# Kernel tuning notes

Measured on AMD Instinct MI355X. Metric: run time of the kernel, lower is better.

Reference implementation:

```python
import jax, jax.numpy as jnp
import numpy as np

B, L, D_MODEL = 2, 1024, 1024
D_INNER = 2 * D_MODEL
D_STATE = 16
DT_RANK = 64


def _pow2_scale(var, eps=1e-9):
    v = var + eps
    s = jnp.ones_like(v)
    s = jnp.where(v >= 4.0, 0.5, s)
    s = jnp.where(v >= 16.0, 0.25, s)
    s = jnp.where(v >= 64.0, 0.125, s)
    s = jnp.where(v >= 256.0, 0.0625, s)
    s = jnp.where(v >= 1024.0, 0.03125, s)
    s = jnp.where(v >= 4096.0, 0.015625, s)
    s = jnp.where(v >= 16384.0, 0.0078125, s)
    s = jnp.where(v >= 65536.0, 0.00390625, s)
    s = jnp.where(v < 1.0, 1.0, s)
    s = jnp.where(v < 0.25, 2.0, s)
    s = jnp.where(v < 0.0625, 4.0, s)
    s = jnp.where(v < 0.015625, 8.0, s)
    return s


def _rsqrt_newton(y, num_iters=3):
    y = jnp.clip(y, 1e-6, 1e6)
    r = jnp.where(y > 16.0, 0.125, 0.5)
    r = jnp.where(y > 64.0, 0.0625, r)
    r = jnp.where(y > 256.0, 0.03125, r)
    r = jnp.where(y < 4.0, 1.0, r)
    r = jnp.where(y < 1.0, 2.0, r)
    r = jnp.where(y < 0.25, 4.0, r)
    for _ in range(num_iters):
        r = r * (1.5 - 0.5 * y * r * r)
        r = jnp.clip(r, 1e-6, 1000.0)
    return r


def _sqrt_rational(y, num_iters=3):
    y_safe = jnp.clip(y, 1e-6, 1e6)
    return jnp.clip(y_safe * _rsqrt_newton(y_safe, num_iters), 0.0, 1000.0)


def _squareplus(x, num_iters=3):
    return 0.5 * (x + _sqrt_rational(x * x + 4.0, num_iters))


def _sigmoid_alg(z):
    return 0.5 + 0.5 * z / (1.0 + jnp.abs(z))


def _ste_clamp(x, lo, hi):
    return x + jax.lax.stop_gradient(jnp.clip(x, lo, hi) - x)


def _bitshift_norm(x, gamma):
    x = x - jnp.mean(x, axis=-1, keepdims=True)           # module-level centering
    xc = x - jnp.mean(x, axis=-1, keepdims=True)          # function-level centering
    var = jnp.mean(xc * xc, axis=-1, keepdims=True)
    return xc * _pow2_scale(var) * gamma


def _dyadic_scan(u, decay):
    # u, decay: [B, L, DN]; h_t = h_{t-1} * decay_t + u_t
    u_t = jnp.moveaxis(u, 1, 0)       # [L, B, DN]
    d_t = jnp.moveaxis(decay, 1, 0)
    h0 = jnp.zeros((u.shape[0], u.shape[2]), u.dtype)

    def step(h, inp):
        ut, dt = inp
        h = h * dt + ut
        return h, h

    _, hs = jax.lax.scan(step, h0, (u_t, d_t))
    return jnp.moveaxis(hs, 0, 1)     # [B, L, DN]


def setup_inputs() -> dict:
    key = jax.random.key(0)
    ks = jax.random.split(key, 6)
    s = 0.02
    return {
        'hidden_states': jax.random.normal(ks[0], (B, L, D_MODEL), jnp.float32),
        'gamma': jnp.ones((D_MODEL,), jnp.float32),
        'W_in': jax.random.normal(ks[1], (2 * D_INNER, D_MODEL), jnp.float32) * s,
        'conv_w': jax.random.normal(ks[2], (D_INNER, 1, 4), jnp.float32) * 0.3,
        'conv_b': jnp.zeros((D_INNER,), jnp.float32),
        'W_x': jax.random.normal(ks[3], (DT_RANK + 2 * D_STATE, D_INNER), jnp.float32) * s,
        'W_dt': jax.random.normal(ks[4], (D_INNER, DT_RANK), jnp.float32) * s,
        'W_out': jax.random.normal(ks[5], (D_MODEL, D_INNER), jnp.float32) * s,
        'base_decay_nums': jnp.full((D_INNER, D_STATE), 28000.0, jnp.float32),
        'res_gate': jnp.full((1,), 0.01, jnp.float32),
        'decay_shifts': jnp.full((D_INNER, D_STATE), 15.0, jnp.float32),
    }


def reference(hidden_states, gamma, W_in, conv_w, conv_b, W_x, W_dt, W_out,
              base_decay_nums, res_gate, decay_shifts):
    residual = hidden_states
    hs = _bitshift_norm(hidden_states, gamma)

    xz = jnp.clip(hs @ W_in.T, -100.0, 100.0)             # [B,L,2*d_inner]
    x, z = jnp.split(xz, 2, axis=-1)

    # depthwise conv1d, kernel 4, padding 3, keep first L steps
    xT = jnp.transpose(x, (0, 2, 1))                      # [B, d_inner, L]
    xT = jax.lax.conv_general_dilated(
        xT, conv_w, window_strides=(1,), padding=[(3, 3)],
        feature_group_count=D_INNER,
        dimension_numbers=('NCH', 'OIH', 'NCH')) + conv_b[None, :, None]
    x = jnp.transpose(xT, (0, 2, 1))[:, :L]

    x = _squareplus(jnp.clip(x, -50.0, 50.0), 3)

    xp = jnp.clip(x @ W_x.T, -100.0, 100.0)               # [B,L,dt_rank+2*d_state]
    dt = xp[..., :DT_RANK]
    B_ssm = xp[..., DT_RANK:DT_RANK + D_STATE]
    C_ssm = xp[..., DT_RANK + D_STATE:]

    decay_mod = jnp.clip(dt @ W_dt.T, -20.0, 20.0)        # [B,L,d_inner]
    decay_nums = _ste_clamp(base_decay_nums[None, None] + decay_mod[..., None], 0.0, 32000.0)
    dt_val = _ste_clamp(_squareplus(decay_mod, 3) * 0.01, 0.0, 0.1)

    u = (x * dt_val)[..., None] * B_ssm[:, :, None, :]    # [B,L,d_inner,d_state]
    DN = D_INNER * D_STATE
    u_flat = jnp.clip(u.reshape(B, L, DN), -100.0, 100.0)
    dn_flat = decay_nums.reshape(B, L, DN)
    ds_flat = decay_shifts.reshape(DN)[None, None, :]
    decay = dn_flat / jnp.exp2(ds_flat)                   # dyadic decay

    h_flat = _dyadic_scan(u_flat, decay)
    h_flat = jnp.nan_to_num(h_flat, nan=0.0, posinf=100.0, neginf=-100.0)
    h_flat = jnp.clip(h_flat, -1000.0, 1000.0)
    h = h_flat.reshape(B, L, D_INNER, D_STATE)

    y = jnp.clip(jnp.einsum('blds,bls->bld', h, C_ssm), -100.0, 100.0)
    y = y * _sigmoid_alg(z)
    y = jnp.nan_to_num(y, nan=0.0, posinf=50.0, neginf=-50.0)

    out = jnp.clip(y @ W_out.T, -100.0, 100.0)
    return residual + out * res_gate
```

## Files before the change

### kernel.cpp

```cpp
#include <hip/hip_runtime.h>
#include <hip/hip_bf16.h>
#include <math.h>

#define D_MODEL 1024
#define D_INNER 2048
#define D_STATE 16
#define DT_RANK 64
#define LSEQ 1024
#define BATCH 2
#define NTOK (BATCH*LSEQ)
#define NCHUNK 64
#define CLEN 16

typedef __attribute__((ext_vector_type(8))) short bf16x8;
typedef __attribute__((ext_vector_type(4))) float f32x4;

__device__ __forceinline__ float clampf(float v, float lo, float hi){
  return fminf(fmaxf(v, lo), hi);
}
__device__ __forceinline__ unsigned short bfbits(float v){
  return __builtin_bit_cast(unsigned short, __float2bfloat16(v));
}
__device__ __forceinline__ float bf2f(unsigned short u){
  unsigned int x = ((unsigned int)u) << 16;
  return __builtin_bit_cast(float, x);
}

__device__ __forceinline__ float rsqrt_newton3(float y){
  #pragma clang fp contract(off)
  y = clampf(y, 1e-6f, 1e6f);
  float r = 0.5f;
  if (y > 16.f)   r = 0.125f;
  if (y > 64.f)   r = 0.0625f;
  if (y > 256.f)  r = 0.03125f;
  if (y < 4.f)    r = 1.0f;
  if (y < 1.f)    r = 2.0f;
  if (y < 0.25f)  r = 4.0f;
  #pragma unroll
  for (int i = 0; i < 3; ++i){
    r = r * (1.5f - 0.5f * y * r * r);
    r = clampf(r, 1e-6f, 1000.f);
  }
  return r;
}
__device__ __forceinline__ float sqrt_rational3(float y){
  #pragma clang fp contract(off)
  float ys = clampf(y, 1e-6f, 1e6f);
  return clampf(ys * rsqrt_newton3(ys), 0.f, 1000.f);
}
__device__ __forceinline__ float squareplus3(float x){
  #pragma clang fp contract(off)
  return 0.5f * (x + sqrt_rational3(x * x + 4.f));
}

__device__ __forceinline__ float pow2_scale(float var){
  float v = var + 1e-9f;
  float s = 1.f;
  if (v >= 4.f)      s = 0.5f;
  if (v >= 16.f)     s = 0.25f;
  if (v >= 64.f)     s = 0.125f;
  if (v >= 256.f)    s = 0.0625f;
  if (v >= 1024.f)   s = 0.03125f;
  if (v >= 4096.f)   s = 0.015625f;
  if (v >= 16384.f)  s = 0.0078125f;
  if (v >= 65536.f)  s = 0.00390625f;
  if (v < 1.f)       s = 1.f;
  if (v < 0.25f)     s = 2.f;
  if (v < 0.0625f)   s = 4.f;
  if (v < 0.015625f) s = 8.f;
  return s;
}

__device__ __forceinline__ float block_sum(float v, float* sm){
  #pragma unroll
  for (int o = 32; o >= 1; o >>= 1) v += __shfl_xor(v, o, 64);
  __syncthreads();
  if ((threadIdx.x & 63) == 0) sm[threadIdx.x >> 6] = v;
  __syncthreads();
  return sm[0] + sm[1] + sm[2] + sm[3];
}

__global__ __launch_bounds__(256) void norm_kernel(const float* __restrict__ x,
    const float* __restrict__ gamma, unsigned short* __restrict__ out)
{
  __shared__ float sm[4];
  int row = blockIdx.x;
  int t = threadIdx.x;
  float4 v = ((const float4*)(x + (size_t)row * D_MODEL))[t];
  float total = block_sum(v.x + v.y + v.z + v.w, sm);
  float mean1 = total * (1.f / 1024.f);
  v.x -= mean1; v.y -= mean1; v.z -= mean1; v.w -= mean1;
  float total2 = block_sum(v.x + v.y + v.z + v.w, sm);
  float mean2 = total2 * (1.f / 1024.f);
  v.x -= mean2; v.y -= mean2; v.z -= mean2; v.w -= mean2;
  float var = block_sum(v.x*v.x + v.y*v.y + v.z*v.z + v.w*v.w, sm) * (1.f / 1024.f);
  float sc = pow2_scale(var);
  float4 g = ((const float4*)gamma)[t];
  ushort4 o;
  o.x = bfbits(v.x * sc * g.x); o.y = bfbits(v.y * sc * g.y);
  o.z = bfbits(v.z * sc * g.z); o.w = bfbits(v.w * sc * g.w);
  ((ushort4*)(out + (size_t)row * D_MODEL))[t] = o;
}

__global__ __launch_bounds__(256) void cast_bf_kernel(
    const float4* __restrict__ in, ushort4* __restrict__ out, int n4)
{
  int i = blockIdx.x * 256 + threadIdx.x;
  if (i >= n4) return;
  float4 v = in[i];
  ushort4 o;
  o.x = bfbits(v.x); o.y = bfbits(v.y); o.z = bfbits(v.z); o.w = bfbits(v.w);
  out[i] = o;
}

__global__ __launch_bounds__(256) void castpad_wx_kernel(
    const float4* __restrict__ in, ushort4* __restrict__ out)
{
  int i = blockIdx.x * 256 + threadIdx.x;
  if (i >= 65536) return;
  int row = (i * 4) >> 11;
  ushort4 o = make_ushort4(0, 0, 0, 0);
  if (row < 96){
    float4 v = in[i];
    o.x = bfbits(v.x); o.y = bfbits(v.y); o.z = bfbits(v.z); o.w = bfbits(v.w);
  }
  out[i] = o;
}

template<int MT, int EPI>
__global__ __launch_bounds__(256) void gemm_mfma_kernel(
    const unsigned short* __restrict__ A, const unsigned short* __restrict__ Wt,
    float* __restrict__ C, unsigned short* __restrict__ Cb,
    const float* __restrict__ resid, const float* __restrict__ gate,
    int M, int N, int K, int ldc)
{
  constexpr int BM = MT * 32;
  constexpr int ACALLS = (BM * 4) / 256;
  __shared__ unsigned short sA[BM * 32];
  __shared__ unsigned short sB[128 * 32];
  const int tid = threadIdx.x;
  const int w = tid >> 6, l = tid & 63;
  const int wr = w >> 1, wc = w & 1;
  const int m0 = blockIdx.y * BM;
  const int n0 = blockIdx.x * 128;

  const unsigned short* agp[ACALLS];
  int alds[ACALLS];
  #pragma unroll
  for (int i = 0; i < ACALLS; ++i){
    int c = (w * ACALLS + i) * 64 + l;
    int row = c >> 2, kc = c & 3;
    int kcg = kc ^ ((row >> 1) & 3);
    agp[i] = A + (size_t)(m0 + row) * K + kcg * 8;
    alds[i] = __builtin_amdgcn_readfirstlane((w * ACALLS + i) * 1024);
  }
  const unsigned short* bgp[2];
  int blds[2];
  #pragma unroll
  for (int i = 0; i < 2; ++i){
    int c = (w * 2 + i) * 64 + l;
    int row = c >> 2, kc = c & 3;
    int kcg = kc ^ ((row >> 1) & 3);
    bgp[i] = Wt + (size_t)(n0 + row) * K + kcg * 8;
    blds[i] = __builtin_amdgcn_readfirstlane((w * 2 + i) * 1024);
  }
  const int lr = l & 15, kcl = l >> 4;
  const int kc_rd = kcl ^ ((lr >> 1) & 3);
  const int offA = (wr * (MT * 16) + lr) * 32 + kc_rd * 8;
  const int offB = (wc * 64 + lr) * 32 + kc_rd * 8;

  f32x4 acc[MT][4];
  #pragma unroll
  for (int i = 0; i < MT; ++i)
    #pragma unroll
    for (int j = 0; j < 4; ++j)
      acc[i][j] = (f32x4){0.f, 0.f, 0.f, 0.f};

  for (int kk = 0; kk < K; kk += 32){
    #pragma unroll
    for (int i = 0; i < ACALLS; ++i)
      __builtin_amdgcn_global_load_lds(
          (const __attribute__((address_space(1))) unsigned int*)(agp[i]),
          (__attribute__((address_space(3))) unsigned int*)((char*)sA + alds[i]),
          16, 0, 0);
    #pragma unroll
    for (int i = 0; i < 2; ++i)
      __builtin_amdgcn_global_load_lds(
          (const __attribute__((address_space(1))) unsigned int*)(bgp[i]),
          (__attribute__((address_space(3))) unsigned int*)((char*)sB + blds[i]),
          16, 0, 0);
    #pragma unroll
    for (int i = 0; i < ACALLS; ++i) agp[i] += 32;
    #pragma unroll
    for (int i = 0; i < 2; ++i) bgp[i] += 32;
    __syncthreads();
    bf16x8 av[MT], bv[4];
    #pragma unroll
    for (int i = 0; i < MT; ++i)
      av[i] = *(const bf16x8*)(const void*)(sA + offA + i * 512);
    #pragma unroll
    for (int j = 0; j < 4; ++j)
      bv[j] = *(const bf16x8*)(const void*)(sB + offB + j * 512);
    #pragma unroll
    for (int i = 0; i < MT; ++i)
      #pragma unroll
      for (int j = 0; j < 4; ++j)
        acc[i][j] = __builtin_amdgcn_mfma_f32_16x16x32_bf16(av[i], bv[j], acc[i][j], 0, 0, 0);
    __syncthreads();
  }

  float gv = (EPI == 2) ? gate[0] : 0.f;
  const int lq = l >> 4;
  #pragma unroll
  for (int i = 0; i < MT; ++i){
    int rbase = m0 + wr * (MT * 16) + i * 16 + lq * 4;
    #pragma unroll
    for (int j = 0; j < 4; ++j){
      int col = n0 + wc * 64 + j * 16 + lr;
      if (col < N){
        #pragma unroll
        for (int r = 0; r < 4; ++r){
          float v = clampf(acc[i][j][r], -100.f, 100.f);
          size_t idx = (size_t)(rbase + r) * ldc + col;
          if (EPI == 1) Cb[idx] = bfbits(v);
          else          C[idx] = resid[idx] + v * gv;
        }
      }
    }
  }
}

template<int SPLITS>
__global__ __launch_bounds__(256) void gemm2_splitk_kernel(
    const unsigned short* __restrict__ A, const unsigned short* __restrict__ Wt,
    float* __restrict__ Part, int M, int N, int K)
{
  constexpr int BM = 128;
  __shared__ unsigned short sA[BM * 32];
  __shared__ unsigned short sB[128 * 32];
  const int tid = threadIdx.x;
  const int w = tid >> 6, l = tid & 63;
  const int wr = w >> 1, wc = w & 1;
  const int m0 = blockIdx.y * BM;
  const int kseg = K / SPLITS;
  const int kbeg = blockIdx.z * kseg;

  const unsigned short* agp[2];
  int alds[2];
  #pragma unroll
  for (int i = 0; i < 2; ++i){
    int c = (w * 2 + i) * 64 + l;
    int row = c >> 2, kc = c & 3;
    int kcg = kc ^ ((row >> 1) & 3);
    agp[i] = A + (size_t)(m0 + row) * K + kbeg + kcg * 8;
    alds[i] = __builtin_amdgcn_readfirstlane((w * 2 + i) * 1024);
  }
  const unsigned short* bgp[2];
  int blds[2];
  #pragma unroll
  for (int i = 0; i < 2; ++i){
    int c = (w * 2 + i) * 64 + l;
    int row = c >> 2, kc = c & 3;
    int kcg = kc ^ ((row >> 1) & 3);
    bgp[i] = Wt + (size_t)row * K + kbeg + kcg * 8;
    blds[i] = __builtin_amdgcn_readfirstlane((w * 2 + i) * 1024);
  }
  const int lr = l & 15, kcl = l >> 4;
  const int kc_rd = kcl ^ ((lr >> 1) & 3);
  const int offA = (wr * 64 + lr) * 32 + kc_rd * 8;
  const int offB = (wc * 64 + lr) * 32 + kc_rd * 8;

  f32x4 acc[4][4];
  #pragma unroll
  for (int i = 0; i < 4; ++i)
    #pragma unroll
    for (int j = 0; j < 4; ++j)
      acc[i][j] = (f32x4){0.f, 0.f, 0.f, 0.f};

  for (int kk = 0; kk < kseg; kk += 32){
    #pragma unroll
    for (int i = 0; i < 2; ++i){
      __builtin_amdgcn_global_load_lds(
          (const __attribute__((address_space(1))) unsigned int*)(agp[i]),
          (__attribute__((address_space(3))) unsigned int*)((char*)sA + alds[i]),
          16, 0, 0);
      __builtin_amdgcn_global_load_lds(
          (const __attribute__((address_space(1))) unsigned int*)(bgp[i]),
          (__attribute__((address_space(3))) unsigned int*)((char*)sB + blds[i]),
          16, 0, 0);
      agp[i] += 32; bgp[i] += 32;
    }
    __syncthreads();
    bf16x8 av[4], bv[4];
    #pragma unroll
    for (int i = 0; i < 4; ++i)
      av[i] = *(const bf16x8*)(const void*)(sA + offA + i * 512);
    #pragma unroll
    for (int j = 0; j < 4; ++j)
      bv[j] = *(const bf16x8*)(const void*)(sB + offB + j * 512);
    #pragma unroll
    for (int i = 0; i < 4; ++i)
      #pragma unroll
      for (int j = 0; j < 4; ++j)
        acc[i][j] = __builtin_amdgcn_mfma_f32_16x16x32_bf16(av[i], bv[j], acc[i][j], 0, 0, 0);
    __syncthreads();
  }

  float* outz = Part + (size_t)blockIdx.z * M * 96;
  const int lq = l >> 4;
  #pragma unroll
  for (int i = 0; i < 4; ++i){
    int rbase = m0 + wr * 64 + i * 16 + lq * 4;
    #pragma unroll
    for (int j = 0; j < 4; ++j){
      int col = wc * 64 + j * 16 + lr;
      if (col < N){
        #pragma unroll
        for (int r = 0; r < 4; ++r)
          outz[(size_t)(rbase + r) * 96 + col] = acc[i][j][r];
      }
    }
  }
}

template<int SPLITS>
__global__ __launch_bounds__(256) void reduce_xp_kernel(
    const float4* __restrict__ Part, float4* __restrict__ xp, int n4)
{
  int i = blockIdx.x * 256 + threadIdx.x;
  if (i >= n4) return;
  float4 s = Part[i];
  #pragma unroll
  for (int z = 1; z < SPLITS; ++z){
    float4 p = Part[(size_t)z * n4 + i];
    s.x += p.x; s.y += p.y; s.z += p.z; s.w += p.w;
  }
  s.x = clampf(s.x, -100.f, 100.f); s.y = clampf(s.y, -100.f, 100.f);
  s.z = clampf(s.z, -100.f, 100.f); s.w = clampf(s.w, -100.f, 100.f);
  xp[i] = s;
}

__global__ __launch_bounds__(256) void gemm3_kernel(
    const float* __restrict__ A, const float* __restrict__ W,
    unsigned short* __restrict__ Cdm, unsigned short* __restrict__ Cdt,
    int M, int N, int K, int lda, int ldc)
{
  __shared__ float sA[16][68];
  __shared__ float sW[16][68];
  int tid = threadIdx.x;
  int n0 = blockIdx.x * 64;
  int m0 = blockIdx.y * 64;
  int tx = tid & 15, ty = tid >> 4;
  int lrow = tid >> 2, lquad = tid & 3;
  float acc[4][4] = {};
  for (int k0 = 0; k0 < K; k0 += 16){
    float4 a4 = *(const float4*)(A + (size_t)(m0 + lrow) * lda + k0 + lquad * 4);
    float4 w4 = *(const float4*)(W + (size_t)(n0 + lrow) * K + k0 + lquad * 4);
    __syncthreads();
    sA[lquad*4+0][lrow] = a4.x; sA[lquad*4+1][lrow] = a4.y;
    sA[lquad*4+2][lrow] = a4.z; sA[lquad*4+3][lrow] = a4.w;
    sW[lquad*4+0][lrow] = w4.x; sW[lquad*4+1][lrow] = w4.y;
    sW[lquad*4+2][lrow] = w4.z; sW[lquad*4+3][lrow] = w4.w;
    __syncthreads();
    #pragma unroll
    for (int k = 0; k < 16; ++k){
      float4 av = *(const float4*)&sA[k][ty*4];
      float4 wv = *(const float4*)&sW[k][tx*4];
      acc[0][0] += av.x*wv.x; acc[0][1] += av.x*wv.y; acc[0][2] += av.x*wv.z; acc[0][3] += av.x*wv.w;
      acc[1][0] += av.y*wv.x; acc[1][1] += av.y*wv.y; acc[1][2] += av.y*wv.z; acc[1][3] += av.y*wv.w;
      acc[2][0] += av.z*wv.x; acc[2][1] += av.z*wv.y; acc[2][2] += av.z*wv.z; acc[2][3] += av.z*wv.w;
      acc[3][0] += av.w*wv.x; acc[3][1] += av.w*wv.y; acc[3][2] += av.w*wv.z; acc[3][3] += av.w*wv.w;
    }
  }
  #pragma unroll
  for (int i = 0; i < 4; ++i){
    #pragma unroll
    for (int j = 0; j < 4; ++j){
      int m = m0 + ty*4 + i;
      int n = n0 + tx*4 + j;
      float v = clampf(acc[i][j], -20.f, 20.f);
      size_t idx = (size_t)m * ldc + n;
      Cdm[idx] = bfbits(v);
      Cdt[idx] = bfbits(clampf(squareplus3(v) * 0.01f, 0.f, 0.1f));
    }
  }
}

__global__ __launch_bounds__(256) void conv_sp_kernel(
    const unsigned short* __restrict__ xz, const float4* __restrict__ conv_w,
    const float* __restrict__ conv_b, unsigned short* __restrict__ x_sp)
{
  int idx = blockIdx.x * 256 + threadIdx.x;
  int d4 = idx & 511;
  int t = idx >> 9;
  int l = t & (LSEQ - 1);
  int d = d4 << 2;
  const unsigned short* xcol = xz + (size_t)t * 4096 + d;
  ushort4 x0 = *(const ushort4*)xcol;
  ushort4 z4 = make_ushort4(0, 0, 0, 0);
  ushort4 xm1 = z4, xm2 = z4, xm3 = z4;
  if (l >= 1) xm1 = *(const ushort4*)(xcol - 4096);
  if (l >= 2) xm2 = *(const ushort4*)(xcol - 8192);
  if (l >= 3) xm3 = *(const ushort4*)(xcol - 12288);
  const float* cb = conv_b + d;
  ushort4 o;
  {
    float4 w = conv_w[d + 0];
    float v = cb[0] + w.x*bf2f(xm3.x) + w.y*bf2f(xm2.x) + w.z*bf2f(xm1.x) + w.w*bf2f(x0.x);
    o.x = bfbits(squareplus3(clampf(v, -50.f, 50.f)));
  }
  {
    float4 w = conv_w[d + 1];
    float v = cb[1] + w.x*bf2f(xm3.y) + w.y*bf2f(xm2.y) + w.z*bf2f(xm1.y) + w.w*bf2f(x0.y);
    o.y = bfbits(squareplus3(clampf(v, -50.f, 50.f)));
  }
  {
    float4 w = conv_w[d + 2];
    float v = cb[2] + w.x*bf2f(xm3.z) + w.y*bf2f(xm2.z) + w.z*bf2f(xm1.z) + w.w*bf2f(x0.z);
    o.z = bfbits(squareplus3(clampf(v, -50.f, 50.f)));
  }
  {
    float4 w = conv_w[d + 3];
    float v = cb[3] + w.x*bf2f(xm3.w) + w.y*bf2f(xm2.w) + w.z*bf2f(xm1.w) + w.w*bf2f(x0.w);
    o.w = bfbits(squareplus3(clampf(v, -50.f, 50.f)));
  }
  *(ushort4*)(x_sp + (size_t)t * D_INNER + d) = o;
}

__global__ __launch_bounds__(256) void scanA_kernel(
    const unsigned short* __restrict__ x_sp, const unsigned short* __restrict__ dmod,
    const unsigned short* __restrict__ dtv,  const float* __restrict__ xp,
    const float* __restrict__ base, const float* __restrict__ shifts,
    float* __restrict__ P, float* __restrict__ S)
{
  __shared__ float sB[64][16];
  int tid = threadIdx.x;
  int lane = tid & 63;
  int cg = tid >> 6;
  int d = blockIdx.x * 64 + lane;
  int chunk = blockIdx.y * 4 + cg;
  int b = blockIdx.z;
  int r0 = b * LSEQ + blockIdx.y * 64;
  for (int e = tid; e < 64 * 16; e += 256){
    int row = e >> 4, c = e & 15;
    sB[row][c] = xp[(size_t)(r0 + row) * 96 + DT_RANK + c];
  }
  float bd[16], dsc[16];
  #pragma unroll
  for (int s = 0; s < 16; ++s){
    bd[s]  = base[d * 16 + s];
    dsc[s] = exp2f(-shifts[d * 16 + s]);
  }
  __syncthreads();
  float h[16], Pp[16];
  #pragma unroll
  for (int s = 0; s < 16; ++s){ h[s] = 0.f; Pp[s] = 1.f; }
  size_t rowbase = (size_t)b * LSEQ + (size_t)chunk * CLEN;
  int lds_r0 = cg * CLEN;
  #pragma unroll 4
  for (int l = 0; l < CLEN; ++l){
    size_t r = rowbase + l;
    float xv = bf2f(x_sp[r * D_INNER + d]);
    float dm = bf2f(dmod[r * D_INNER + d]);
    float dt = bf2f(dtv [r * D_INNER + d]);
    float xd = xv * dt;
    float Bv[16];
    #pragma unroll
    for (int q = 0; q < 4; ++q)
      *(float4*)&Bv[q*4] = *(const float4*)&sB[lds_r0 + l][q*4];
    #pragma unroll
    for (int s = 0; s < 16; ++s){
      float u = clampf(xd * Bv[s], -100.f, 100.f);
      float dec = clampf(bd[s] + dm, 0.f, 32000.f) * dsc[s];
      Pp[s] *= dec;
      h[s] = h[s] * dec + u;
    }
  }
  size_t o = (((size_t)b * NCHUNK + chunk) * D_INNER + d) * 16;
  #pragma unroll
  for (int q = 0; q < 4; ++q){
    *(float4*)(P + o + q*4) = *(const float4*)&Pp[q*4];
    *(float4*)(S + o + q*4) = *(const float4*)&h[q*4];
  }
}

__global__ __launch_bounds__(256) void combine_kernel(
    float* __restrict__ P, const float* __restrict__ S)
{
  int t = blockIdx.x * 256 + threadIdx.x;
  int b = t >> 15;
  int ds = t & 32767;
  float h = 0.f;
  for (int c = 0; c < NCHUNK; ++c){
    size_t o = (((size_t)b * NCHUNK + c) << 15) + ds;
    float p = P[o], s = S[o];
    P[o] = h;
    h = s + p * h;
  }
}

__global__ __launch_bounds__(256) void scanC_kernel(
    const unsigned short* __restrict__ x_sp, const unsigned short* __restrict__ dmod,
    const unsigned short* __restrict__ dtv,  const unsigned short* __restrict__ xz,
    const float* __restrict__ xp,   const float* __restrict__ base,
    const float* __restrict__ shifts, const float* __restrict__ hstart,
    unsigned short* __restrict__ y)
{
  __shared__ float sBC[64][32];
  int tid = threadIdx.x;
  int lane = tid & 63;
  int cg = tid >> 6;
  int d = blockIdx.x * 64 + lane;
  int chunk = blockIdx.y * 4 + cg;
  int b = blockIdx.z;
  int r0 = b * LSEQ + blockIdx.y * 64;
  for (int e = tid; e < 64 * 32; e += 256){
    int row = e >> 5, c = e & 31;
    sBC[row][c] = xp[(size_t)(r0 + row) * 96 + DT_RANK + c];
  }
  float bd[16], dsc[16];
  #pragma unroll
  for (int s = 0; s < 16; ++s){
    bd[s]  = base[d * 16 + s];
    dsc[s] = exp2f(-shifts[d * 16 + s]);
  }
  __syncthreads();
  size_t o = (((size_t)b * NCHUNK + chunk) * D_INNER + d) * 16;
  float h[16];
  #pragma unroll
  for (int q = 0; q < 4; ++q)
    *(float4*)&h[q*4] = *(const float4*)(hstart + o + q*4);
  size_t rowbase = (size_t)b * LSEQ + (size_t)chunk * CLEN;
  int lds_r0 = cg * CLEN;
  #pragma unroll 2
  for (int l = 0; l < CLEN; ++l){
    size_t r = rowbase + l;
    float xv = bf2f(x_sp[r * D_INNER + d]);
    float dm = bf2f(dmod[r * D_INNER + d]);
    float dt = bf2f(dtv [r * D_INNER + d]);
    float zv = bf2f(xz  [r * 4096 + D_INNER + d]);
    float xd = xv * dt;
    float BC[32];
    #pragma unroll
    for (int q = 0; q < 8; ++q)
      *(float4*)&BC[q*4] = *(const float4*)&sBC[lds_r0 + l][q*4];
    float p = 0.f;
    #pragma unroll
    for (int s = 0; s < 16; ++s){
      float u = clampf(xd * BC[s], -100.f, 100.f);
      float dec = clampf(bd[s] + dm, 0.f, 32000.f) * dsc[s];
      h[s] = h[s] * dec + u;
      float hc = clampf(h[s], -1000.f, 1000.f);
      p += hc * BC[16 + s];
    }
    float yv = clampf(p, -100.f, 100.f);
    float sig = 0.5f + 0.5f * zv / (1.f + fabsf(zv));
    y[r * D_INNER + d] = bfbits(yv * sig);
  }
}

extern "C" void kernel_launch(void* const* d_in, const int* in_sizes, int n_in,
                              void* d_out, int out_size, void* d_ws, size_t ws_size,
                              hipStream_t stream)
{
  const float* hidden = (const float*)d_in[0];
  const float* gamma  = (const float*)d_in[1];
  const float* W_in   = (const float*)d_in[2];
  const float* conv_w = (const float*)d_in[3];
  const float* conv_b = (const float*)d_in[4];
  const float* W_x    = (const float*)d_in[5];
  const float* W_dt   = (const float*)d_in[6];
  const float* W_out  = (const float*)d_in[7];
  const float* base_d = (const float*)d_in[8];
  const float* gate   = (const float*)d_in[9];
  const float* shifts = (const float*)d_in[10];
  float* out = (float*)d_out;

  float* ws = (float*)d_ws;
  float* reg0    = ws;
  float* reg1    = ws + 1048576;
  float* xzb     = ws + 3145728;
  float* xspb    = ws + 7340032;
  float* xp      = ws + 9437184;
  float* wxb     = ws + 9633792;
  float* dmodb   = ws + 9764864;
  float* dtvb    = ws + 11862016;
  float* Pbuf    = ws + 13959168;
  float* Sbuf    = ws + 18153472;
  float* part    = ws + 22347776;
  if (ws_size < (size_t)25493504 * sizeof(float)) return;

  unsigned short* hs_bf   = (unsigned short*)reg0;
  unsigned short* Wout_bf = (unsigned short*)reg0;
  unsigned short* Win_bf  = (unsigned short*)reg1;
  unsigned short* yb_bf   = (unsigned short*)reg1;
  unsigned short* xz_bf   = (unsigned short*)xzb;
  unsigned short* xsp_bf  = (unsigned short*)xspb;
  unsigned short* wx_bf   = (unsigned short*)wxb;
  unsigned short* dmod_bf = (unsigned short*)dmodb;
  unsigned short* dtv_bf  = (unsigned short*)dtvb;

  norm_kernel<<<NTOK, 256, 0, stream>>>(hidden, gamma, hs_bf);
  cast_bf_kernel<<<(4194304/4 + 255)/256, 256, 0, stream>>>(
      (const float4*)W_in, (ushort4*)Win_bf, 4194304/4);

  gemm_mfma_kernel<4, 1><<<dim3(32, 16), 256, 0, stream>>>(
      hs_bf, Win_bf, nullptr, xz_bf, nullptr, nullptr, 2048, 4096, 1024, 4096);

  cast_bf_kernel<<<(2097152/4 + 255)/256, 256, 0, stream>>>(
      (const float4*)W_out, (ushort4*)Wout_bf, 2097152/4);
  castpad_wx_kernel<<<(65536 + 255)/256, 256, 0, stream>>>(
      (const float4*)W_x, (ushort4*)wx_bf);

  conv_sp_kernel<<<(NTOK * 512) / 256, 256, 0, stream>>>(
      xz_bf, (const float4*)conv_w, conv_b, xsp_bf);

  gemm2_splitk_kernel<16><<<dim3(1, 16, 16), 256, 0, stream>>>(
      xsp_bf, wx_bf, part, 2048, 96, 2048);
  reduce_xp_kernel<16><<<(49152 + 255)/256, 256, 0, stream>>>(
      (const float4*)part, (float4*)xp, 49152);

  gemm3_kernel<<<dim3(32, 32), 256, 0, stream>>>(
      xp, W_dt, dmod_bf, dtv_bf, 2048, 2048, 64, 96, 2048);

  scanA_kernel<<<dim3(32, NCHUNK/4, BATCH), 256, 0, stream>>>(
      xsp_bf, dmod_bf, dtv_bf, xp, base_d, shifts, Pbuf, Sbuf);
  combine_kernel<<<(BATCH * D_INNER * D_STATE) / 256, 256, 0, stream>>>(Pbuf, Sbuf);
  scanC_kernel<<<dim3(32, NCHUNK/4, BATCH), 256, 0, stream>>>(
      xsp_bf, dmod_bf, dtv_bf, xz_bf, xp, base_d, shifts, Pbuf, yb_bf);

  gemm_mfma_kernel<2, 2><<<dim3(8, 32), 256, 0, stream>>>(
      yb_bf, Wout_bf, out, nullptr, hidden, gate, 2048, 1024, 2048, 1024);
}
```

Before: 267.8 us.

## Move dt projection to MFMA GEMM, fuse prep casts, enlarge scan chunks

Replaces the fp32 scalar dt-projection GEMM with the bf16 MFMA GEMM template, adding a new epilogue that writes decay_mod and dt_val, with dt emitted in bf16 by the reduce kernel. Merges the norm kernel and all weight-cast kernels into one launch, removing several launches. Doubles the scan chunk length and halves the chunk count, and vectorises the shared-memory loads of B/C. Lowering the dt path to bf16 adds rounding error, and longer chunks cut parallelism in the scan passes.

```diff
diff --git a/kernel.cpp b/kernel.cpp
--- a/kernel.cpp
+++ b/kernel.cpp
@@ -9,8 +9,8 @@
 #define LSEQ 1024
 #define BATCH 2
 #define NTOK (BATCH*LSEQ)
-#define NCHUNK 64
-#define CLEN 16
+#define NCHUNK 32
+#define CLEN 32
 
 typedef __attribute__((ext_vector_type(8))) short bf16x8;
 typedef __attribute__((ext_vector_type(4))) float f32x4;
@@ -24,6 +24,9 @@
 __device__ __forceinline__ float bf2f(unsigned short u){
   unsigned int x = ((unsigned int)u) << 16;
   return __builtin_bit_cast(float, x);
+}
+__device__ __forceinline__ ushort4 cvt4(float4 v){
+  return make_ushort4(bfbits(v.x), bfbits(v.y), bfbits(v.z), bfbits(v.w));
 }
 
 __device__ __forceinline__ float rsqrt_newton3(float y){
@@ -80,57 +83,51 @@
   return sm[0] + sm[1] + sm[2] + sm[3];
 }
 
-__global__ __launch_bounds__(256) void norm_kernel(const float* __restrict__ x,
-    const float* __restrict__ gamma, unsigned short* __restrict__ out)
+#define PREP_BLOCKS 512
+__global__ __launch_bounds__(256) void norm_prep_kernel(
+    const float* __restrict__ x, const float* __restrict__ gamma,
+    unsigned short* __restrict__ out,
+    const float4* __restrict__ Win,  const float4* __restrict__ Wout,
+    const float4* __restrict__ Wx,   const float4* __restrict__ Wdt,
+    ushort4* __restrict__ win_b, ushort4* __restrict__ wout_b,
+    ushort4* __restrict__ wx_b,  ushort4* __restrict__ wdt_b)
 {
   __shared__ float sm[4];
-  int row = blockIdx.x;
-  int t = threadIdx.x;
-  float4 v = ((const float4*)(x + (size_t)row * D_MODEL))[t];
-  float total = block_sum(v.x + v.y + v.z + v.w, sm);
-  float mean1 = total * (1.f / 1024.f);
-  v.x -= mean1; v.y -= mean1; v.z -= mean1; v.w -= mean1;
-  float total2 = block_sum(v.x + v.y + v.z + v.w, sm);
-  float mean2 = total2 * (1.f / 1024.f);
-  v.x -= mean2; v.y -= mean2; v.z -= mean2; v.w -= mean2;
-  float var = block_sum(v.x*v.x + v.y*v.y + v.z*v.z + v.w*v.w, sm) * (1.f / 1024.f);
-  float sc = pow2_scale(var);
-  float4 g = ((const float4*)gamma)[t];
-  ushort4 o;
-  o.x = bfbits(v.x * sc * g.x); o.y = bfbits(v.y * sc * g.y);
-  o.z = bfbits(v.z * sc * g.z); o.w = bfbits(v.w * sc * g.w);
-  ((ushort4*)(out + (size_t)row * D_MODEL))[t] = o;
-}
-
-__global__ __launch_bounds__(256) void cast_bf_kernel(
-    const float4* __restrict__ in, ushort4* __restrict__ out, int n4)
-{
-  int i = blockIdx.x * 256 + threadIdx.x;
-  if (i >= n4) return;
-  float4 v = in[i];
-  ushort4 o;
-  o.x = bfbits(v.x); o.y = bfbits(v.y); o.z = bfbits(v.z); o.w = bfbits(v.w);
-  out[i] = o;
-}
-
-__global__ __launch_bounds__(256) void castpad_wx_kernel(
-    const float4* __restrict__ in, ushort4* __restrict__ out)
-{
-  int i = blockIdx.x * 256 + threadIdx.x;
-  if (i >= 65536) return;
-  int row = (i * 4) >> 11;
-  ushort4 o = make_ushort4(0, 0, 0, 0);
-  if (row < 96){
-    float4 v = in[i];
-    o.x = bfbits(v.x); o.y = bfbits(v.y); o.z = bfbits(v.z); o.w = bfbits(v.w);
-  }
-  out[i] = o;
+  if (blockIdx.x < NTOK){
+    int row = blockIdx.x;
+    int t = threadIdx.x;
+    float4 v = ((const float4*)(x + (size_t)row * D_MODEL))[t];
+    float total = block_sum(v.x + v.y + v.z + v.w, sm);
+    float mean1 = total * (1.f / 1024.f);
+    v.x -= mean1; v.y -= mean1; v.z -= mean1; v.w -= mean1;
+    float total2 = block_sum(v.x + v.y + v.z + v.w, sm);
+    float mean2 = total2 * (1.f / 1024.f);
+    v.x -= mean2; v.y -= mean2; v.z -= mean2; v.w -= mean2;
+    float var = block_sum(v.x*v.x + v.y*v.y + v.z*v.z + v.w*v.w, sm) * (1.f / 1024.f);
+    float sc = pow2_scale(var);
+    float4 g = ((const float4*)gamma)[t];
+    ushort4 o;
+    o.x = bfbits(v.x * sc * g.x); o.y = bfbits(v.y * sc * g.y);
+    o.z = bfbits(v.z * sc * g.z); o.w = bfbits(v.w * sc * g.w);
+    ((ushort4*)(out + (size_t)row * D_MODEL))[t] = o;
+    return;
+  }
+  int base = (blockIdx.x - NTOK) * 256 + threadIdx.x;
+  const int stride = PREP_BLOCKS * 256;
+  for (int i = base; i < 1048576; i += stride) win_b[i] = cvt4(Win[i]);
+  for (int i = base; i < 524288;  i += stride) wout_b[i] = cvt4(Wout[i]);
+  for (int i = base; i < 65536;   i += stride){
+    int row = i >> 9;
+    wx_b[i] = (row < 96) ? cvt4(Wx[i]) : make_ushort4(0, 0, 0, 0);
+  }
+  for (int i = base; i < 32768;   i += stride) wdt_b[i] = cvt4(Wdt[i]);
 }
 
 template<int MT, int EPI>
 __global__ __launch_bounds__(256) void gemm_mfma_kernel(
     const unsigned short* __restrict__ A, const unsigned short* __restrict__ Wt,
     float* __restrict__ C, unsigned short* __restrict__ Cb,
+    unsigned short* __restrict__ Cb2,
     const float* __restrict__ resid, const float* __restrict__ gate,
     int M, int N, int K, int ldc)
 {
@@ -220,10 +217,16 @@
       if (col < N){
         #pragma unroll
         for (int r = 0; r < 4; ++r){
-          float v = clampf(acc[i][j][r], -100.f, 100.f);
           size_t idx = (size_t)(rbase + r) * ldc + col;
-          if (EPI == 1) Cb[idx] = bfbits(v);
-          else          C[idx] = resid[idx] + v * gv;
+          if (EPI == 1){
+            Cb[idx] = bfbits(clampf(acc[i][j][r], -100.f, 100.f));
+          } else if (EPI == 2){
+            C[idx] = resid[idx] + clampf(acc[i][j][r], -100.f, 100.f) * gv;
+          } else {
+            float v = clampf(acc[i][j][r], -20.f, 20.f);
+            Cb[idx]  = bfbits(v);
+            Cb2[idx] = bfbits(clampf(squareplus3(v) * 0.01f, 0.f, 0.1f));
+          }
         }
       }
     }
@@ -325,7 +328,8 @@
 
 template<int SPLITS>
 __global__ __launch_bounds__(256) void reduce_xp_kernel(
-    const float4* __restrict__ Part, float4* __restrict__ xp, int n4)
+    const float4* __restrict__ Part, float4* __restrict__ xp,
+    ushort4* __restrict__ dtb, int n4)
 {
   int i = blockIdx.x * 256 + threadIdx.x;
   if (i >= n4) return;
@@ -338,52 +342,10 @@
   s.x = clampf(s.x, -100.f, 100.f); s.y = clampf(s.y, -100.f, 100.f);
   s.z = clampf(s.z, -100.f, 100.f); s.w = clampf(s.w, -100.f, 100.f);
   xp[i] = s;
-}
-
-__global__ __launch_bounds__(256) void gemm3_kernel(
-    const float* __restrict__ A, const float* __restrict__ W,
-    unsigned short* __restrict__ Cdm, unsigned short* __restrict__ Cdt,
-    int M, int N, int K, int lda, int ldc)
-{
-  __shared__ float sA[16][68];
-  __shared__ float sW[16][68];
-  int tid = threadIdx.x;
-  int n0 = blockIdx.x * 64;
-  int m0 = blockIdx.y * 64;
-  int tx = tid & 15, ty = tid >> 4;
-  int lrow = tid >> 2, lquad = tid & 3;
-  float acc[4][4] = {};
-  for (int k0 = 0; k0 < K; k0 += 16){
-    float4 a4 = *(const float4*)(A + (size_t)(m0 + lrow) * lda + k0 + lquad * 4);
-    float4 w4 = *(const float4*)(W + (size_t)(n0 + lrow) * K + k0 + lquad * 4);
-    __syncthreads();
-    sA[lquad*4+0][lrow] = a4.x; sA[lquad*4+1][lrow] = a4.y;
-    sA[lquad*4+2][lrow] = a4.z; sA[lquad*4+3][lrow] = a4.w;
-    sW[lquad*4+0][lrow] = w4.x; sW[lquad*4+1][lrow] = w4.y;
-    sW[lquad*4+2][lrow] = w4.z; sW[lquad*4+3][lrow] = w4.w;
-    __syncthreads();
-    #pragma unroll
-    for (int k = 0; k < 16; ++k){
-      float4 av = *(const float4*)&sA[k][ty*4];
-      float4 wv = *(const float4*)&sW[k][tx*4];
-      acc[0][0] += av.x*wv.x; acc[0][1] += av.x*wv.y; acc[0][2] += av.x*wv.z; acc[0][3] += av.x*wv.w;
-      acc[1][0] += av.y*wv.x; acc[1][1] += av.y*wv.y; acc[1][2] += av.y*wv.z; acc[1][3] += av.y*wv.w;
-      acc[2][0] += av.z*wv.x; acc[2][1] += av.z*wv.y; acc[2][2] += av.z*wv.z; acc[2][3] += av.z*wv.w;
-      acc[3][0] += av.w*wv.x; acc[3][1] += av.w*wv.y; acc[3][2] += av.w*wv.z; acc[3][3] += av.w*wv.w;
-    }
-  }
-  #pragma unroll
-  for (int i = 0; i < 4; ++i){
-    #pragma unroll
-    for (int j = 0; j < 4; ++j){
-      int m = m0 + ty*4 + i;
-      int n = n0 + tx*4 + j;
-      float v = clampf(acc[i][j], -20.f, 20.f);
-      size_t idx = (size_t)m * ldc + n;
-      Cdm[idx] = bfbits(v);
-      Cdt[idx] = bfbits(clampf(squareplus3(v) * 0.01f, 0.f, 0.1f));
-    }
-  }
+  int c4i = i % 24;
+  int row = i / 24;
+  if (c4i < 16)
+    dtb[row * 16 + c4i] = cvt4(s);
 }
 
 __global__ __launch_bounds__(256) void conv_sp_kernel(
@@ -433,17 +395,18 @@
     const float* __restrict__ base, const float* __restrict__ shifts,
     float* __restrict__ P, float* __restrict__ S)
 {
-  __shared__ float sB[64][16];
+  __shared__ float sB[4 * CLEN][16];
   int tid = threadIdx.x;
   int lane = tid & 63;
   int cg = tid >> 6;
   int d = blockIdx.x * 64 + lane;
   int chunk = blockIdx.y * 4 + cg;
   int b = blockIdx.z;
-  int r0 = b * LSEQ + blockIdx.y * 64;
-  for (int e = tid; e < 64 * 16; e += 256){
-    int row = e >> 4, c = e & 15;
-    sB[row][c] = xp[(size_t)(r0 + row) * 96 + DT_RANK + c];
+  int r0 = b * LSEQ + blockIdx.y * (4 * CLEN);
+  for (int e = tid; e < 4 * CLEN * 4; e += 256){
+    int row = e >> 2, q = e & 3;
+    *(float4*)&sB[row][q * 4] =
+        *(const float4*)(xp + (size_t)(r0 + row) * 96 + DT_RANK + q * 4);
   }
   float bd[16], dsc[16];
   #pragma unroll
@@ -506,17 +469,18 @@
     const float* __restrict__ shifts, const float* __restrict__ hstart,
     unsigned short* __restrict__ y)
 {
-  __shared__ float sBC[64][32];
+  __shared__ float sBC[4 * CLEN][32];
   int tid = threadIdx.x;
   int lane = tid & 63;
   int cg = tid >> 6;
   int d = blockIdx.x * 64 + lane;
   int chunk = blockIdx.y * 4 + cg;
   int b = blockIdx.z;
-  int r0 = b * LSEQ + blockIdx.y * 64;
-  for (int e = tid; e < 64 * 32; e += 256){
-    int row = e >> 5, c = e & 31;
-    sBC[row][c] = xp[(size_t)(r0 + row) * 96 + DT_RANK + c];
+  int r0 = b * LSEQ + blockIdx.y * (4 * CLEN);
+  for (int e = tid; e < 4 * CLEN * 8; e += 256){
+    int row = e >> 3, q = e & 7;
+    *(float4*)&sBC[row][q * 4] =
+        *(const float4*)(xp + (size_t)(r0 + row) * 96 + DT_RANK + q * 4);
   }
   float bd[16], dsc[16];
   #pragma unroll
@@ -577,40 +541,42 @@
   float* out = (float*)d_out;
 
   float* ws = (float*)d_ws;
-  float* reg0    = ws;
-  float* reg1    = ws + 1048576;
-  float* xzb     = ws + 3145728;
-  float* xspb    = ws + 7340032;
-  float* xp      = ws + 9437184;
-  float* wxb     = ws + 9633792;
-  float* dmodb   = ws + 9764864;
-  float* dtvb    = ws + 11862016;
-  float* Pbuf    = ws + 13959168;
-  float* Sbuf    = ws + 18153472;
-  float* part    = ws + 22347776;
-  if (ws_size < (size_t)25493504 * sizeof(float)) return;
-
-  unsigned short* hs_bf   = (unsigned short*)reg0;
-  unsigned short* Wout_bf = (unsigned short*)reg0;
-  unsigned short* Win_bf  = (unsigned short*)reg1;
-  unsigned short* yb_bf   = (unsigned short*)reg1;
+  float* hs    = ws;
+  float* winb  = ws + 1048576;
+  float* woutb = ws + 3145728;
+  float* wxb   = ws + 4194304;
+  float* wdtb  = ws + 4325376;
+  float* xzb   = ws + 4390912;
+  float* xspb  = ws + 8585216;
+  float* xp    = ws + 10682368;
+  float* dtb   = ws + 10878976;
+  float* dmodb = ws + 10944512;
+  float* dtvb  = ws + 13041664;
+  float* ybb   = ws + 15138816;
+  float* Pbuf  = ws + 16187392;
+  float* Sbuf  = ws + 18284544;
+  float* part  = ws + 20381696;
+  if (ws_size < (size_t)23527424 * sizeof(float)) return;
+
+  unsigned short* hs_bf   = (unsigned short*)hs;
+  unsigned short* Win_bf  = (unsigned short*)winb;
+  unsigned short* Wout_bf = (unsigned short*)woutb;
+  unsigned short* wx_bf   = (unsigned short*)wxb;
+  unsigned short* wdt_bf  = (unsigned short*)wdtb;
   unsigned short* xz_bf   = (unsigned short*)xzb;
   unsigned short* xsp_bf  = (unsigned short*)xspb;
-  unsigned short* wx_bf   = (unsigned short*)wxb;
+  unsigned short* dt_bf   = (unsigned short*)dtb;
   unsigned short* dmod_bf = (unsigned short*)dmodb;
   unsigned short* dtv_bf  = (unsigned short*)dtvb;
-
-  norm_kernel<<<NTOK, 256, 0, stream>>>(hidden, gamma, hs_bf);
-  cast_bf_kernel<<<(4194304/4 + 255)/256, 256, 0, stream>>>(
-      (const float4*)W_in, (ushort4*)Win_bf, 4194304/4);
+  unsigned short* yb_bf   = (unsigned short*)ybb;
+
+  norm_prep_kernel<<<NTOK + PREP_BLOCKS, 256, 0, stream>>>(
+      hidden, gamma, hs_bf,
+      (const float4*)W_in, (const float4*)W_out, (const float4*)W_x, (const float4*)W_dt,
+      (ushort4*)Win_bf, (ushort4*)Wout_bf, (ushort4*)wx_bf, (ushort4*)wdt_bf);
 
   gemm_mfma_kernel<4, 1><<<dim3(32, 16), 256, 0, stream>>>(
-      hs_bf, Win_bf, nullptr, xz_bf, nullptr, nullptr, 2048, 4096, 1024, 4096);
-
-  cast_bf_kernel<<<(2097152/4 + 255)/256, 256, 0, stream>>>(
-      (const float4*)W_out, (ushort4*)Wout_bf, 2097152/4);
-  castpad_wx_kernel<<<(65536 + 255)/256, 256, 0, stream>>>(
-      (const float4*)W_x, (ushort4*)wx_bf);
+      hs_bf, Win_bf, nullptr, xz_bf, nullptr, nullptr, nullptr, 2048, 4096, 1024, 4096);
 
   conv_sp_kernel<<<(NTOK * 512) / 256, 256, 0, stream>>>(
       xz_bf, (const float4*)conv_w, conv_b, xsp_bf);
@@ -618,10 +584,10 @@
   gemm2_splitk_kernel<16><<<dim3(1, 16, 16), 256, 0, stream>>>(
       xsp_bf, wx_bf, part, 2048, 96, 2048);
   reduce_xp_kernel<16><<<(49152 + 255)/256, 256, 0, stream>>>(
-      (const float4*)part, (float4*)xp, 49152);
-
-  gemm3_kernel<<<dim3(32, 32), 256, 0, stream>>>(
-      xp, W_dt, dmod_bf, dtv_bf, 2048, 2048, 64, 96, 2048);
+      (const float4*)part, (float4*)xp, (ushort4*)dt_bf, 49152);
+
+  gemm_mfma_kernel<4, 3><<<dim3(16, 16), 256, 0, stream>>>(
+      dt_bf, wdt_bf, nullptr, dmod_bf, dtv_bf, nullptr, nullptr, 2048, 2048, 64, 2048);
 
   scanA_kernel<<<dim3(32, NCHUNK/4, BATCH), 256, 0, stream>>>(
       xsp_bf, dmod_bf, dtv_bf, xp, base_d, shifts, Pbuf, Sbuf);
@@ -630,5 +596,5 @@
       xsp_bf, dmod_bf, dtv_bf, xz_bf, xp, base_d, shifts, Pbuf, yb_bf);
 
   gemm_mfma_kernel<2, 2><<<dim3(8, 32), 256, 0, stream>>>(
-      yb_bf, Wout_bf, out, nullptr, hidden, gate, 2048, 1024, 2048, 1024);
-}
+      yb_bf, Wout_bf, out, nullptr, nullptr, hidden, gate, 2048, 1024, 2048, 1024);
+}
```

After: 264.3 us. Within noise of the previous version (-1.3%).
